# Performance work log

Hardware: AMD Instinct MI355X
Metric: run time of the kernel (lower is better)

## Reference

```python
import jax, jax.numpy as jnp
import numpy as np

B, S, DIN, H, N, L_S4, L_RES, ED = 512, 500, 14, 128, 256, 4, 6, 256


def setup_inputs() -> dict:
    key = jax.random.key(0)
    ks = jax.random.split(key, 32)
    f = jnp.float32
    rn = lambda k, sh, s: jax.random.normal(k, sh, f) * s
    inp = {
        'x': rn(ks[0], (B, S, DIN), 1.0),
        'timesteps': jax.random.randint(ks[1], (B,), 0, 1000),
        'mask': (jax.random.uniform(ks[2], (B, S, 1)) < 0.9).astype(f),
        'observed': rn(ks[3], (B, S, DIN), 1.0),
        'W_in': rn(ks[4], (DIN, H), DIN ** -0.5), 'b_in': jnp.zeros((H,), f),
        'time_W1': rn(ks[5], (ED, 2 * H), ED ** -0.5), 'time_b1': jnp.zeros((2 * H,), f),
        'time_W2': rn(ks[6], (2 * H, H), (2 * H) ** -0.5), 'time_b2': jnp.zeros((H,), f),
        's4_ln_g': jnp.ones((L_S4, H), f), 's4_ln_b': jnp.zeros((L_S4, H), f),
        's4_logA': jnp.log(0.5 * jnp.ones((L_S4, H, N), f)),
        's4_Aim': jnp.broadcast_to(np.pi * jnp.arange(N, dtype=f), (L_S4, H, N)).copy(),
        's4_Cre': rn(ks[7], (L_S4, H, N), 0.5 ** 0.5),
        's4_Cim': rn(ks[8], (L_S4, H, N), 0.5 ** 0.5),
        's4_D': rn(ks[9], (L_S4, H), 1.0),
        's4_logdt': jax.random.uniform(ks[10], (L_S4, H), f, np.log(0.001), np.log(0.1)),
        's4_Wo': rn(ks[11], (L_S4, H, H), H ** -0.5), 's4_bo': jnp.zeros((L_S4, H), f),
        'res_ln_g': jnp.ones((L_RES, H), f), 'res_ln_b': jnp.zeros((L_RES, H), f),
        'res_W1': rn(ks[12], (L_RES, H, 2 * H), H ** -0.5), 'res_b1': jnp.zeros((L_RES, 2 * H), f),
        'res_W2': rn(ks[13], (L_RES, 2 * H, H), (2 * H) ** -0.5), 'res_b2': jnp.zeros((L_RES, H), f),
        'W_out': rn(ks[14], (H, DIN), H ** -0.5), 'b_out': jnp.zeros((DIN,), f),
    }
    return inp


def _ln(x, g, b):
    m = x.mean(-1, keepdims=True)
    v = ((x - m) ** 2).mean(-1, keepdims=True)
    return (x - m) * jax.lax.rsqrt(v + 1e-5) * g + b


def reference(x, timesteps, mask, observed, W_in, b_in, time_W1, time_b1, time_W2,
              time_b2, s4_ln_g, s4_ln_b, s4_logA, s4_Aim, s4_Cre, s4_Cim, s4_D,
              s4_logdt, s4_Wo, s4_bo, res_ln_g, res_ln_b, res_W1, res_b1, res_W2,
              res_b2, W_out, b_out):
    Bb, Ss, _ = x.shape
    Hh = W_in.shape[1]
    x_cond = x * mask + observed
    # sinusoidal positional encoding gated by mask -> [B,S,H]
    pos = jnp.arange(Ss, dtype=jnp.float32)
    div = jnp.exp(-jnp.log(10000.0) * 2.0 * jnp.arange(Hh // 2, dtype=jnp.float32) / Hh)
    ang = pos[:, None] * div
    pe = jnp.concatenate([jnp.sin(ang), jnp.cos(ang)], -1)  # [S,H]
    h = x_cond @ W_in + b_in + pe[None] * mask
    # S4D layers: prenorm -> FFT causal conv with Vandermonde kernel -> GELU -> proj -> residual
    t_idx = jnp.arange(Ss, dtype=jnp.float32)
    for l in range(s4_logA.shape[0]):
        z = _ln(h, s4_ln_g[l], s4_ln_b[l])
        dt = jnp.exp(s4_logdt[l])[:, None]                       # [H,1]
        A = -jnp.exp(s4_logA[l]) + 1j * s4_Aim[l]                # [H,N]
        dtA = dt * A
        C = (s4_Cre[l] + 1j * s4_Cim[l]) * (jnp.exp(dtA) - 1.0) / A
        V = jnp.exp(dtA[:, :, None] * t_idx)                     # [H,N,S]
        K = 2.0 * jnp.einsum('hn,hnl->hl', C, V).real            # [H,S]
        u = jnp.transpose(z, (0, 2, 1))                          # [B,H,S]
        n = 2 * Ss
        y = jnp.fft.irfft(jnp.fft.rfft(u, n) * jnp.fft.rfft(K, n), n)[..., :Ss]
        y = y + s4_D[l][None, :, None] * u
        y = jax.nn.gelu(jnp.transpose(y, (0, 2, 1)), approximate=False)
        h = h + y @ s4_Wo[l] + s4_bo[l]
    # diffusion time embedding
    half = time_W1.shape[0] // 2
    emb = jnp.log(10000.0) / (half - 1)
    freqs = jnp.exp(-emb * jnp.arange(half, dtype=jnp.float32))
    te = timesteps.astype(jnp.float32)[:, None] * freqs
    te = jnp.concatenate([jnp.sin(te), jnp.cos(te)], -1)
    te = jax.nn.silu(te @ time_W1 + time_b1) @ time_W2 + time_b2
    h = h + te[:, None, :]
    # residual MLP blocks
    for l in range(res_W1.shape[0]):
        z = _ln(h, res_ln_g[l], res_ln_b[l])
        h = h + jax.nn.gelu(z @ res_W1[l] + res_b1[l], approximate=False) @ res_W2[l] + res_b2[l]
    return h @ W_out + b_out
```

## Files before the change

### kernel.cpp

```cpp
#include <hip/hip_runtime.h>
#include <math.h>

#define B_ 512
#define S_ 500
#define SP_ 512
#define DIN_ 14
#define H_ 128
#define N_ 256
#define NT_ 256000

#define SWZ(r) ((((r) ^ ((r) >> 4)) & 15) << 4)

typedef __attribute__((ext_vector_type(8))) short short8v;
typedef __attribute__((ext_vector_type(4))) float f32x4;

__device__ __forceinline__ float gelu_f(float x) {
    float y = 0.7978845608028654f * x * (1.0f + 0.044715f * x * x);
    float t = 1.0f - __fdividef(2.0f, 1.0f + __expf(2.0f * y));
    return 0.5f * x * (1.0f + t);
}
__device__ __forceinline__ short f2bf(float f) {
    unsigned u = __builtin_bit_cast(unsigned, f);
    u += 0x7fffu + ((u >> 16) & 1u);
    return (short)(u >> 16);
}
__device__ __forceinline__ float bf2f(short s) {
    return __builtin_bit_cast(float, ((unsigned)(unsigned short)s) << 16);
}

__global__ __launch_bounds__(256) void k_kmat(
    const float* __restrict__ logA, const float* __restrict__ Aim,
    const float* __restrict__ Cre, const float* __restrict__ Cim,
    const float* __restrict__ logdt, float* __restrict__ Km)
{
    int lh = blockIdx.x;
    __shared__ float sCr[256], sCi[256], sAr[256], sAif[256];
    {
        int n = threadIdx.x;
        int idx = lh * N_ + n;
        double dt  = exp((double)logdt[lh]);
        double Are = -exp((double)logA[idx]);
        double Aiv = (double)Aim[idx];
        double ar  = dt * Are, ai = dt * Aiv;
        double er  = exp(ar);
        double E1r = er * cos(ai) - 1.0, E1i = er * sin(ai);
        double inv = 1.0 / (Are * Are + Aiv * Aiv);
        double qR  = (E1r * Are + E1i * Aiv) * inv;
        double qI  = (E1i * Are - E1r * Aiv) * inv;
        double cre = (double)Cre[idx], cim = (double)Cim[idx];
        sCr[n] = (float)(cre * qR - cim * qI);
        sCi[n] = (float)(cre * qI + cim * qR);
        sAr[n] = (float)ar;
        sAif[n] = (float)fmod(ai, 6.283185307179586476925286766559);
    }
    __syncthreads();
    for (int s = threadIdx.x; s < SP_; s += 256) {
        float acc = 0.0f;
        if (s < S_) {
            float fs = (float)s;
            for (int n = 0; n < N_; ++n) {
                float er = __expf(sAr[n] * fs);
                float y = sAif[n] * fs;
                y -= 6.28318530717958648f * rintf(y * 0.159154943091895336f);
                float sn, cs; __sincosf(y, &sn, &cs);
                acc = fmaf(er * sCr[n], cs, acc);
                acc = fmaf(-er * sCi[n], sn, acc);
            }
            acc *= 2.0f;
        }
        Km[lh * SP_ + s] = acc;
    }
}

__global__ __launch_bounds__(256) void k_toep(
    const float* __restrict__ Kl, short* __restrict__ Tblk)
{
    int hh = blockIdx.x, d = blockIdx.y;
    const float* Kr = Kl + hh * SP_;
    short* Tb = Tblk + (((size_t)hh * 4 + d) << 14);
    int base = d * 128;
    for (int i = threadIdx.x; i < 16384; i += 256) {
        int s = i >> 7, t = i & 127;
        int diff = base + s - t;
        float v = (diff >= 0 && diff < S_) ? Kr[diff] : 0.f;
        Tb[i] = f2bf(v);
    }
}

__global__ __launch_bounds__(128) void k_petab(float* __restrict__ pet)
{
    int s = blockIdx.x, j = threadIdx.x;
    int jj = j & 63;
    float dv = expf(-0.14391156831212787f * (float)jj);
    float ang = (float)s * dv;
    pet[s * 128 + j] = (j < 64) ? sinf(ang) : cosf(ang);
}

__global__ __launch_bounds__(256) void k_inproj(
    const float* __restrict__ x, const float* __restrict__ mask,
    const float* __restrict__ obs, const float* __restrict__ Win,
    const float* __restrict__ bin, const float* __restrict__ pet,
    float* __restrict__ h, float2* __restrict__ st)
{
    int wid = threadIdx.x >> 6, lane = threadIdx.x & 63;
    int tok0 = blockIdx.x * 16 + wid * 4;
    float w0[DIN_], w1[DIN_];
#pragma unroll
    for (int d = 0; d < DIN_; ++d) {
        w0[d] = Win[d * H_ + lane];
        w1[d] = Win[d * H_ + lane + 64];
    }
    float b0 = bin[lane], b1 = bin[lane + 64];
    for (int t = 0; t < 4; ++t) {
        int tok = tok0 + t;
        int s = tok % S_;
        float m = mask[tok];
        float a0 = b0, a1 = b1;
        const float* xp = x + (size_t)tok * DIN_;
        const float* op = obs + (size_t)tok * DIN_;
#pragma unroll
        for (int d = 0; d < DIN_; ++d) {
            float xc = xp[d] * m + op[d];
            a0 += xc * w0[d];
            a1 += xc * w1[d];
        }
        float h0 = a0 + pet[s * 128 + lane] * m;
        float h1 = a1 + pet[s * 128 + lane + 64] * m;
        float s1 = h0 + h1, s2 = h0 * h0 + h1 * h1;
#pragma unroll
        for (int off = 32; off > 0; off >>= 1) {
            s1 += __shfl_xor(s1, off, 64);
            s2 += __shfl_xor(s2, off, 64);
        }
        float mu = s1 * 0.0078125f;
        float rs = rsqrtf(s2 * 0.0078125f - mu * mu + 1e-5f);
        if (lane == 0) st[tok] = make_float2(mu, rs);
        h[(size_t)tok * H_ + lane] = h0;
        h[(size_t)tok * H_ + lane + 64] = h1;
    }
}

__global__ __launch_bounds__(256) void k_temb(
    const int* __restrict__ ts, const float* __restrict__ W1,
    const float* __restrict__ b1, const float* __restrict__ W2,
    const float* __restrict__ b2, float* __restrict__ te)
{
    __shared__ float feat[256];
    __shared__ float mid[256];
    int b = blockIdx.x, j = threadIdx.x;
    float t = (float)ts[b];
    float fr = expf(-0.07252236513367075f * (float)(j & 127));
    float ang = t * fr;
    feat[j] = (j < 128) ? sinf(ang) : cosf(ang);
    __syncthreads();
    float acc = b1[j];
    for (int k = 0; k < 256; ++k) acc += feat[k] * W1[k * 256 + j];
    mid[j] = acc / (1.0f + expf(-acc));
    __syncthreads();
    if (j < 128) {
        float a2 = b2[j];
        for (int k = 0; k < 256; ++k) a2 += mid[k] * W2[k * 128 + j];
        te[b * 128 + j] = a2;
    }
}

__global__ __launch_bounds__(256) void k_wcast(
    const float* __restrict__ Wo, const float* __restrict__ rW1,
    const float* __restrict__ rW2,
    short* __restrict__ WoT, short* __restrict__ W1T, short* __restrict__ W2T)
{
    int i = blockIdx.x * 256 + threadIdx.x;
    if (i < 65536) {
        int l = i >> 14, r = i & 16383, n = r >> 7, k = r & 127;
        WoT[i] = f2bf(Wo[(size_t)(l * 128 + k) * 128 + n]);
    } else if (i < 262144) {
        int j = i - 65536;
        int l = j >> 15, r = j & 32767, n = r >> 7, k = r & 127;
        W1T[j] = f2bf(rW1[(size_t)(l * 128 + k) * 256 + n]);
    } else if (i < 458752) {
        int j = i - 262144;
        int l = j >> 15, r = j & 32767, n = r >> 8, k = r & 255;
        W2T[j] = f2bf(rW2[(size_t)(l * 256 + k) * 128 + n]);
    }
}

__global__ __launch_bounds__(256) void k_ln_tb(
    const float* __restrict__ h, const float2* __restrict__ stc,
    const float* __restrict__ g, const float* __restrict__ be,
    short* __restrict__ ubt)
{
    int b = blockIdx.x, s0 = blockIdx.y * 64;
    int ntok = min(64, S_ - s0);
    __shared__ float tile[64 * 129];
    __shared__ float mu_[64], rs_[64];
    for (int idx = threadIdx.x; idx < (ntok << 7); idx += 256) {
        int i = idx >> 7, k = idx & 127;
        tile[i * 129 + k] = h[(size_t)(b * S_ + s0 + i) * H_ + k];
    }
    if (threadIdx.x < ntok) {
        float2 ms = stc[(size_t)b * S_ + s0 + threadIdx.x];
        mu_[threadIdx.x] = ms.x; rs_[threadIdx.x] = ms.y;
    }
    __syncthreads();
    for (int idx = threadIdx.x; idx < 128 * 32; idx += 256) {
        int k = idx >> 5, i = (idx & 31) * 2;
        float v0 = (i < ntok)     ? (tile[i * 129 + k]       - mu_[i])     * rs_[i]     * g[k] + be[k] : 0.f;
        float v1 = (i + 1 < ntok) ? (tile[(i + 1) * 129 + k] - mu_[i + 1]) * rs_[i + 1] * g[k] + be[k] : 0.f;
        unsigned lo = (unsigned short)f2bf(v0);
        unsigned hi = (unsigned short)f2bf(v1);
        *(unsigned*)(ubt + ((size_t)b * H_ + k) * SP_ + s0 + i) = lo | (hi << 16);
    }
}

__global__ __launch_bounds__(256) void k_cgemm(
    const short* __restrict__ ubt, const short* __restrict__ Tblk,
    const float* __restrict__ D, short* __restrict__ ybt)
{
    __shared__ short As[16384];
    __shared__ short Bs[16384];
    int hh = blockIdx.x, si = blockIdx.y, bt = blockIdx.z;
    int tid = threadIdx.x;
    int lane = tid & 63, wid = tid >> 6;
    int wm = wid >> 1, wn = wid & 1;
    int fr = lane & 15, ko = (lane >> 4) << 3;
    const short* Ab = ubt + ((size_t)(bt * 128) * H_ + hh) * SP_;

    f32x4 acc[4][4];
    f32x4 zv = {0.f, 0.f, 0.f, 0.f};
#pragma unroll
    for (int m = 0; m < 4; ++m)
#pragma unroll
        for (int n = 0; n < 4; ++n) acc[m][n] = zv;

    for (int tj = 0; tj <= si; ++tj) {
        if (tj) __syncthreads();
        const short* Bb = Tblk + (((size_t)hh * 4 + (si - tj)) << 14);
#pragma unroll
        for (int p = 0; p < 8; ++p) {
            int idx = p * 256 + tid;
            int row = idx >> 4, c16 = idx & 15;
            int byt = row * 256 + ((c16 * 16) ^ SWZ(row));
            *(short8v*)((char*)As + byt) =
                *(const short8v*)(Ab + (size_t)row * (H_ * SP_) + tj * 128 + c16 * 8);
            *(short8v*)((char*)Bs + byt) =
                *(const short8v*)(Bb + row * 128 + c16 * 8);
        }
        __syncthreads();
#pragma unroll
        for (int ks = 0; ks < 4; ++ks) {
            short8v a[4], b[4];
#pragma unroll
            for (int m = 0; m < 4; ++m) {
                int row = wm * 64 + m * 16 + fr;
                int byt = row * 256 + (((ks * 32 + ko) * 2) ^ SWZ(row));
                a[m] = *(const short8v*)((const char*)As + byt);
            }
#pragma unroll
            for (int n = 0; n < 4; ++n) {
                int row = wn * 64 + n * 16 + fr;
                int byt = row * 256 + (((ks * 32 + ko) * 2) ^ SWZ(row));
                b[n] = *(const short8v*)((const char*)Bs + byt);
            }
#pragma unroll
            for (int m = 0; m < 4; ++m)
#pragma unroll
                for (int n = 0; n < 4; ++n)
                    acc[m][n] = __builtin_amdgcn_mfma_f32_16x16x32_bf16(
                        a[m], b[n], acc[m][n], 0, 0, 0);
        }
        if (tj < si) __syncthreads();
    }

    float Dh = D[hh];
#pragma unroll
    for (int m = 0; m < 4; ++m) {
        int b0 = wm * 64 + m * 16 + (lane >> 4) * 4;
#pragma unroll
        for (int n = 0; n < 4; ++n) {
            int sC = si * 128 + wn * 64 + n * 16 + fr;
#pragma unroll
            for (int j = 0; j < 4; ++j) {
                int bg = bt * 128 + b0 + j;
                size_t off = ((size_t)bg * H_ + hh) * SP_ + sC;
                float u = bf2f(ubt[off]);
                ybt[off] = f2bf(gelu_f(acc[m][n][j] + Dh * u));
            }
        }
    }
}

__global__ __launch_bounds__(256) void k_p4(
    const short* __restrict__ ybt, const short* __restrict__ BT,
    const float* __restrict__ bias, const float* __restrict__ te,
    float* __restrict__ hres, float2* __restrict__ st,
    short* __restrict__ un, const float* __restrict__ gn,
    const float* __restrict__ bn)
{
    __shared__ __align__(16) char smem[65536];
    int tid = threadIdx.x;
    int bm = blockIdx.x;
    int bl = bm >> 2, s0t = (bm & 3) * 128;
    int lane = tid & 63, wid = tid >> 6;
    int wm = wid >> 1, wn = wid & 1;
    int fr = lane & 15, ko = (lane >> 4) << 3;

    f32x4 acc[4][4];
    f32x4 zv = {0.f, 0.f, 0.f, 0.f};
#pragma unroll
    for (int m = 0; m < 4; ++m)
#pragma unroll
        for (int n = 0; n < 4; ++n) acc[m][n] = zv;

    const short* Yb = ybt + ((size_t)bl << 16);
#pragma unroll
    for (int p = 0; p < 8; ++p) {
        int idx = p * 256 + tid;
        int hh = idx >> 4, sc = idx & 15;
        short8v y = *(const short8v*)(Yb + (size_t)hh * 512 + s0t + sc * 8);
#pragma unroll
        for (int e = 0; e < 8; ++e) {
            int row = sc * 8 + e;
            int byt = row * 256 + ((hh * 2) ^ SWZ(row));
            *(short*)(smem + byt) = y[e];
        }
    }
#pragma unroll
    for (int p = 0; p < 8; ++p) {
        int idx = p * 256 + tid;
        int row = idx >> 4, c16 = idx & 15;
        int byt = row * 256 + ((c16 * 16) ^ SWZ(row));
        *(short8v*)(smem + 32768 + byt) =
            *(const short8v*)(BT + (size_t)row * 128 + c16 * 8);
    }
    __syncthreads();
#pragma unroll
    for (int ks = 0; ks < 4; ++ks) {
        short8v a[4], b[4];
#pragma unroll
        for (int m = 0; m < 4; ++m) {
            int row = wm * 64 + m * 16 + fr;
            int byt = row * 256 + (((ks * 32 + ko) * 2) ^ SWZ(row));
            a[m] = *(const short8v*)(smem + byt);
        }
#pragma unroll
        for (int n = 0; n < 4; ++n) {
            int row = wn * 64 + n * 16 + fr;
            int byt = row * 256 + (((ks * 32 + ko) * 2) ^ SWZ(row));
            b[n] = *(const short8v*)(smem + 32768 + byt);
        }
#pragma unroll
        for (int m = 0; m < 4; ++m)
#pragma unroll
            for (int n = 0; n < 4; ++n)
                acc[m][n] = __builtin_amdgcn_mfma_f32_16x16x32_bf16(
                    a[m], b[n], acc[m][n], 0, 0, 0);
    }

    float* red = (float*)smem;
    short* znT = (short*)(smem + 32768);
    __syncthreads();
#pragma unroll
    for (int m = 0; m < 4; ++m) {
#pragma unroll
        for (int j = 0; j < 4; ++j) {
            int rl = wm * 64 + m * 16 + (lane >> 4) * 4 + j;
            int R = bm * 128 + rl;
            int b_ = R >> 9, s = R & 511;
            bool valid = (s < S_);
            float s1 = 0.f, s2 = 0.f;
#pragma unroll
            for (int n = 0; n < 4; ++n) {
                int C = wn * 64 + n * 16 + fr;
                float v = 0.f;
                if (valid) {
                    float t = te ? te[b_ * 128 + C] : 0.f;
                    size_t go = ((size_t)b_ * S_ + s) * 128 + C;
                    v = hres[go] + acc[m][n][j] + bias[C] + t;
                    hres[go] = v;
                }
                acc[m][n][j] = v;
                s1 += v; s2 += v * v;
            }
            s1 += __shfl_xor(s1, 1, 64); s2 += __shfl_xor(s2, 1, 64);
            s1 += __shfl_xor(s1, 2, 64); s2 += __shfl_xor(s2, 2, 64);
            s1 += __shfl_xor(s1, 4, 64); s2 += __shfl_xor(s2, 4, 64);
            s1 += __shfl_xor(s1, 8, 64); s2 += __shfl_xor(s2, 8, 64);
            if (fr == 0) {
                red[(wn * 128 + rl) * 2]     = s1;
                red[(wn * 128 + rl) * 2 + 1] = s2;
            }
        }
    }
    __syncthreads();
#pragma unroll
    for (int m = 0; m < 4; ++m) {
#pragma unroll
        for (int j = 0; j < 4; ++j) {
            int rl = wm * 64 + m * 16 + (lane >> 4) * 4 + j;
            int R = bm * 128 + rl;
            int b_ = R >> 9, s = R & 511;
            bool valid = (s < S_);
            float s1 = red[rl * 2]     + red[(128 + rl) * 2];
            float s2 = red[rl * 2 + 1] + red[(128 + rl) * 2 + 1];
            float mu = s1 * 0.0078125f;
            float rs = rsqrtf(s2 * 0.0078125f - mu * mu + 1e-5f);
            if (valid && fr == 0 && wn == 0)
                st[(size_t)b_ * S_ + s] = make_float2(mu, rs);
            if (un) {
#pragma unroll
                for (int n = 0; n < 4; ++n) {
                    int C = wn * 64 + n * 16 + fr;
                    float z = valid ? (acc[m][n][j] - mu) * rs * gn[C] + bn[C] : 0.f;
                    *(short*)((char*)znT + C * 256 + ((rl * 2) ^ SWZ(C))) = f2bf(z);
                }
            }
        }
    }
    if (un) {
        __syncthreads();
#pragma unroll
        for (int p = 0; p < 8; ++p) {
            int idx = p * 256 + tid;
            int C = idx >> 4, rlg = idx & 15;
            short8v z8 = *(const short8v*)((const char*)znT + C * 256 + ((rlg * 16) ^ SWZ(C)));
            *(short8v*)(un + (((size_t)(bl * 128 + C)) << 9) + s0t + rlg * 8) = z8;
        }
    }
}

__global__ __launch_bounds__(512) void k_mlp(
    float* hres, const float2* __restrict__ st,
    const short* __restrict__ W1T, const float* __restrict__ rb1,
    const short* __restrict__ W2T, const float* __restrict__ rb2,
    const float* __restrict__ g6, const float* __restrict__ b6)
{
    __shared__ __align__(16) char As1[32768];
    __shared__ __align__(16) char BsA[32768];
    int tid = threadIdx.x;
    int lane = tid & 63, wid = tid >> 6;
    int wm = wid >> 1, wn = wid & 1;
    int fr = lane & 15, ko = (lane >> 4) << 3;
    int q4 = (lane >> 4) * 4;
    size_t tok0 = (size_t)blockIdx.x * 128;

    f32x4 v[2][4];
#pragma unroll
    for (int m = 0; m < 2; ++m) {
#pragma unroll
        for (int j = 0; j < 4; ++j) {
            int rl = wm * 32 + m * 16 + q4 + j;
            float2 ms = st[tok0 + rl];
            const float* hp = hres + (tok0 + rl) * 128;
#pragma unroll
            for (int n = 0; n < 4; ++n) {
                int C = wn * 64 + n * 16 + fr;
                float hv = hp[C];
                v[m][n][j] = hv;
                float z = (hv - ms.x) * ms.y * g6[C] + b6[C];
                int byt = rl * 256 + ((C * 2) ^ SWZ(rl));
                *(short*)(As1 + byt) = f2bf(z);
            }
        }
    }

    for (int l = 0; l < 6; ++l) {
        const short* W1 = W1T + l * 32768;
        const short* W2 = W2T + l * 32768;
        const float* b1 = rb1 + l * 256;
        const float* b2 = rb2 + l * 128;

        f32x4 acc1[2][8];
        f32x4 zvv = {0.f, 0.f, 0.f, 0.f};
#pragma unroll
        for (int m = 0; m < 2; ++m)
#pragma unroll
            for (int n = 0; n < 8; ++n) acc1[m][n] = zvv;

#pragma unroll
        for (int gy = 0; gy < 2; ++gy) {
#pragma unroll
            for (int p = 0; p < 4; ++p) {
                int idx = p * 512 + tid;
                int row = idx >> 4, c16 = idx & 15;
                int byt = row * 256 + ((c16 * 16) ^ SWZ(row));
                *(short8v*)(BsA + byt) =
                    *(const short8v*)(W1 + (size_t)(gy * 128 + row) * 128 + c16 * 8);
            }
            __syncthreads();
#pragma unroll
            for (int ks = 0; ks < 4; ++ks) {
                short8v a[2], b[4];
#pragma unroll
                for (int m = 0; m < 2; ++m) {
                    int row = wm * 32 + m * 16 + fr;
                    int byt = row * 256 + (((ks * 32 + ko) * 2) ^ SWZ(row));
                    a[m] = *(const short8v*)(As1 + byt);
                }
#pragma unroll
                for (int n = 0; n < 4; ++n) {
                    int row = wn * 64 + n * 16 + fr;
                    int byt = row * 256 + (((ks * 32 + ko) * 2) ^ SWZ(row));
                    b[n] = *(const short8v*)(BsA + byt);
                }
#pragma unroll
                for (int m = 0; m < 2; ++m)
#pragma unroll
                    for (int n = 0; n < 4; ++n)
                        acc1[m][gy * 4 + n] = __builtin_amdgcn_mfma_f32_16x16x32_bf16(
                            a[m], b[n], acc1[m][gy * 4 + n], 0, 0, 0);
            }
            __syncthreads();
        }

        f32x4 acc2[2][4];
#pragma unroll
        for (int m = 0; m < 2; ++m)
#pragma unroll
            for (int n = 0; n < 4; ++n) acc2[m][n] = zvv;
#pragma unroll
        for (int kk = 0; kk < 2; ++kk) {
#pragma unroll
            for (int m = 0; m < 2; ++m) {
#pragma unroll
                for (int j = 0; j < 4; ++j) {
                    int rl = wm * 32 + m * 16 + q4 + j;
#pragma unroll
                    for (int n = 0; n < 4; ++n) {
                        int c = wn * 64 + n * 16 + fr;
                        float y1 = gelu_f(acc1[m][kk * 4 + n][j] + b1[kk * 128 + c]);
                        int byt = rl * 256 + ((c * 2) ^ SWZ(rl));
                        *(short*)(As1 + byt) = f2bf(y1);
                    }
                }
            }
#pragma unroll
            for (int p = 0; p < 4; ++p) {
                int idx = p * 512 + tid;
                int row = idx >> 4, c16 = idx & 15;
                int byt = row * 256 + ((c16 * 16) ^ SWZ(row));
                *(short8v*)(BsA + byt) =
                    *(const short8v*)(W2 + (size_t)row * 256 + kk * 128 + c16 * 8);
            }
            __syncthreads();
#pragma unroll
            for (int ks = 0; ks < 4; ++ks) {
                short8v a[2], b[4];
#pragma unroll
                for (int m = 0; m < 2; ++m) {
                    int row = wm * 32 + m * 16 + fr;
                    int byt = row * 256 + (((ks * 32 + ko) * 2) ^ SWZ(row));
                    a[m] = *(const short8v*)(As1 + byt);
                }
#pragma unroll
                for (int n = 0; n < 4; ++n) {
                    int row = wn * 64 + n * 16 + fr;
                    int byt = row * 256 + (((ks * 32 + ko) * 2) ^ SWZ(row));
                    b[n] = *(const short8v*)(BsA + byt);
                }
#pragma unroll
                for (int m = 0; m < 2; ++m)
#pragma unroll
                    for (int n = 0; n < 4; ++n)
                        acc2[m][n] = __builtin_amdgcn_mfma_f32_16x16x32_bf16(
                            a[m], b[n], acc2[m][n], 0, 0, 0);
            }
            __syncthreads();
        }

#pragma unroll
        for (int m = 0; m < 2; ++m)
#pragma unroll
            for (int n = 0; n < 4; ++n) {
                float bj = b2[wn * 64 + n * 16 + fr];
#pragma unroll
                for (int j = 0; j < 4; ++j)
                    v[m][n][j] += acc2[m][n][j] + bj;
            }
        if (l < 5) {
            float* red = (float*)BsA;
#pragma unroll
            for (int m = 0; m < 2; ++m) {
#pragma unroll
                for (int j = 0; j < 4; ++j) {
                    int rl = wm * 32 + m * 16 + q4 + j;
                    float s1 = 0.f, s2 = 0.f;
#pragma unroll
                    for (int n = 0; n < 4; ++n) {
                        float t = v[m][n][j];
                        s1 += t; s2 += t * t;
                    }
                    s1 += __shfl_xor(s1, 1, 64); s2 += __shfl_xor(s2, 1, 64);
                    s1 += __shfl_xor(s1, 2, 64); s2 += __shfl_xor(s2, 2, 64);
                    s1 += __shfl_xor(s1, 4, 64); s2 += __shfl_xor(s2, 4, 64);
                    s1 += __shfl_xor(s1, 8, 64); s2 += __shfl_xor(s2, 8, 64);
                    if (fr == 0) {
                        red[(wn * 128 + rl) * 2]     = s1;
                        red[(wn * 128 + rl) * 2 + 1] = s2;
                    }
                }
            }
            __syncthreads();
            const float* gl = g6 + (l + 1) * 128;
            const float* bl2 = b6 + (l + 1) * 128;
#pragma unroll
            for (int m = 0; m < 2; ++m) {
#pragma unroll
                for (int j = 0; j < 4; ++j) {
                    int rl = wm * 32 + m * 16 + q4 + j;
                    float s1 = red[rl * 2]     + red[(128 + rl) * 2];
                    float s2 = red[rl * 2 + 1] + red[(128 + rl) * 2 + 1];
                    float mu = s1 * 0.0078125f;
                    float rs = rsqrtf(s2 * 0.0078125f - mu * mu + 1e-5f);
#pragma unroll
                    for (int n = 0; n < 4; ++n) {
                        int C = wn * 64 + n * 16 + fr;
                        float z = (v[m][n][j] - mu) * rs * gl[C] + bl2[C];
                        int byt = rl * 256 + ((C * 2) ^ SWZ(rl));
                        *(short*)(As1 + byt) = f2bf(z);
                    }
                }
            }
            __syncthreads();
        }
    }

#pragma unroll
    for (int m = 0; m < 2; ++m) {
#pragma unroll
        for (int j = 0; j < 4; ++j) {
            int rl = wm * 32 + m * 16 + q4 + j;
            float* hp = hres + (tok0 + rl) * 128;
#pragma unroll
            for (int n = 0; n < 4; ++n)
                hp[wn * 64 + n * 16 + fr] = v[m][n][j];
        }
    }
}

__global__ __launch_bounds__(256) void k_out(
    const float* __restrict__ h, const float* __restrict__ Wout,
    const float* __restrict__ bout, float* __restrict__ out)
{
    __shared__ float wt[16 * 132];
    __shared__ float tile[64 * 132];
    int tok0 = blockIdx.x * 64;
    for (int idx = threadIdx.x; idx < 2048; idx += 256) {
        int j = idx >> 7, k = idx & 127;
        wt[j * 132 + k] = (j < 14) ? Wout[k * 14 + j] : 0.f;
    }
    const float4* hp = (const float4*)(h + (size_t)tok0 * 128);
    for (int idx = threadIdx.x; idx < 2048; idx += 256) {
        int row = idx >> 5, c4 = idx & 31;
        *((float4*)(tile + row * 132) + c4) = hp[idx];
    }
    __syncthreads();
    int i = threadIdx.x >> 2, jq = threadIdx.x & 3;
    float aj[4] = {0.f, 0.f, 0.f, 0.f};
    const float4* tr = (const float4*)(tile + i * 132);
#pragma unroll 8
    for (int kk = 0; kk < 32; ++kk) {
        float4 hv = tr[kk];
#pragma unroll
        for (int r = 0; r < 4; ++r) {
            float4 wv = *((const float4*)(wt + (jq * 4 + r) * 132) + kk);
            aj[r] += hv.x * wv.x + hv.y * wv.y + hv.z * wv.z + hv.w * wv.w;
        }
    }
#pragma unroll
    for (int r = 0; r < 4; ++r) {
        int j = jq * 4 + r;
        if (j < 14)
            out[(size_t)(tok0 + i) * 14 + j] = aj[r] + bout[j];
    }
}

extern "C" void kernel_launch(void* const* d_in, const int* in_sizes, int n_in,
                              void* d_out, int out_size, void* d_ws, size_t ws_size,
                              hipStream_t stream)
{
    (void)in_sizes; (void)n_in; (void)out_size;
    const float* x      = (const float*)d_in[0];
    const int*   tsteps = (const int*)  d_in[1];
    const float* mask   = (const float*)d_in[2];
    const float* obs    = (const float*)d_in[3];
    const float* Win    = (const float*)d_in[4];
    const float* bin    = (const float*)d_in[5];
    const float* tW1    = (const float*)d_in[6];
    const float* tb1    = (const float*)d_in[7];
    const float* tW2    = (const float*)d_in[8];
    const float* tb2    = (const float*)d_in[9];
    const float* lng4   = (const float*)d_in[10];
    const float* lnb4   = (const float*)d_in[11];
    const float* logA   = (const float*)d_in[12];
    const float* Aim    = (const float*)d_in[13];
    const float* Cre    = (const float*)d_in[14];
    const float* Cim    = (const float*)d_in[15];
    const float* Dp     = (const float*)d_in[16];
    const float* logdt  = (const float*)d_in[17];
    const float* Wo     = (const float*)d_in[18];
    const float* bo     = (const float*)d_in[19];
    const float* lng6   = (const float*)d_in[20];
    const float* lnb6   = (const float*)d_in[21];
    const float* rW1    = (const float*)d_in[22];
    const float* rb1    = (const float*)d_in[23];
    const float* rW2    = (const float*)d_in[24];
    const float* rb2    = (const float*)d_in[25];
    const float* Woutp  = (const float*)d_in[26];
    const float* boutp  = (const float*)d_in[27];

    float*  ws  = (float*)d_ws;
    float*  h   = ws;
    float*  Km  = h + 32768000;
    float*  te  = Km + 262144;
    float2* st  = (float2*)(te + 65536);
    float*  pet = (float*)st + 512000;
    short*  WoT = (short*)(pet + 64000);
    short*  W1T = WoT + 65536;
    short*  W2T = W1T + 196608;
    float*  big = (float*)(W2T + 196608);
    size_t  wf  = ws_size / sizeof(float);
    size_t  fixed = 33901056;
    size_t  avail = (wf > fixed) ? (wf - fixed) : 0;

    bool flowA = (avail >= 29360128);

    k_kmat<<<512, 256, 0, stream>>>(logA, Aim, Cre, Cim, logdt, Km);
    k_petab<<<S_, 128, 0, stream>>>(pet);
    k_inproj<<<NT_ / 16, 256, 0, stream>>>(x, mask, obs, Win, bin, pet, h, st);
    k_temb<<<B_, 256, 0, stream>>>(tsteps, tW1, tb1, tW2, tb2, te);
    k_wcast<<<1792, 256, 0, stream>>>(Wo, rW1, rW2, WoT, W1T, W2T);

    if (flowA) {
        short* ubtA = (short*)big;
        short* ubtB = ubtA + 16777216;
        short* ybt  = ubtB + 16777216;
        short* Tblk = ybt + 16777216;

        k_ln_tb<<<dim3(256, 8), 256, 0, stream>>>(h, st, lng4, lnb4, ubtA);
        k_ln_tb<<<dim3(256, 8), 256, 0, stream>>>(
            h + (size_t)256 * S_ * H_, st + (size_t)256 * S_, lng4, lnb4, ubtB);

        for (int l = 0; l < 4; ++l) {
            k_toep<<<dim3(H_, 4), 256, 0, stream>>>(Km + (size_t)l * H_ * SP_, Tblk);
            for (int cb = 0; cb < 2; ++cb) {
                size_t bOff = (size_t)cb * 256;
                float* hb = h + bOff * S_ * H_;
                short* ub = cb ? ubtB : ubtA;
                const float* tep = (l == 3) ? (te + bOff * H_) : (const float*)0;
                short* un = (l < 3) ? ub : (short*)0;
                k_cgemm<<<dim3(H_, 4, 2), 256, 0, stream>>>(ub, Tblk, Dp + l * H_, ybt);
                k_p4<<<1024, 256, 0, stream>>>(
                    ybt, WoT + l * 16384, bo + l * H_, tep, hb, st + bOff * S_,
                    un, lng4 + (l + 1) * H_, lnb4 + (l + 1) * H_);
            }
        }
    } else {
        int CHB = 64;
        for (int c = 256; c >= 64; c >>= 1)
            if ((size_t)c * 65536 + 4194304 <= avail) { CHB = c; break; }
        short* ubt  = (short*)big;
        short* ybt  = ubt + (size_t)CHB * 65536;
        short* Tblk = ybt + (size_t)CHB * 65536;
        int nCB = B_ / CHB;
        for (int l = 0; l < 4; ++l) {
            k_toep<<<dim3(H_, 4), 256, 0, stream>>>(Km + (size_t)l * H_ * SP_, Tblk);
            for (int cb = 0; cb < nCB; ++cb) {
                size_t bOff = (size_t)cb * CHB;
                float* hb = h + bOff * S_ * H_;
                const float* tep = (l == 3) ? (te + bOff * H_) : (const float*)0;
                k_ln_tb<<<dim3(CHB, 8), 256, 0, stream>>>(
                    hb, st + bOff * S_, lng4 + l * H_, lnb4 + l * H_, ubt);
                k_cgemm<<<dim3(H_, 4, CHB / 128), 256, 0, stream>>>(
                    ubt, Tblk, Dp + l * H_, ybt);
                k_p4<<<CHB * 4, 256, 0, stream>>>(
                    ybt, WoT + l * 16384, bo + l * H_, tep, hb, st + bOff * S_,
                    (short*)0, lng4, lnb4);
            }
        }
    }

    k_mlp<<<NT_ / 128, 512, 0, stream>>>(h, st, W1T, rb1, W2T, rb2, lng6, lnb6);

    k_out<<<NT_ / 64, 256, 0, stream>>>(h, Woutp, boutp, (float*)d_out);
}
```

Measured before the change: 2.078 ms.

## Swap MFMA operand roles in residual MLP so each lane owns contiguous features

The residual MLP kernel now feeds weights as the A operand and tokens as the B operand of the MFMA. Each lane's accumulator then holds four consecutive feature columns for one token. This allows vectorised float4 global loads and stores of the residual state, short4 LDS writes of the LayerNorm and GELU outputs, and float4 loads of biases and LN parameters, replacing scattered scalar accesses. The LN row reduction shrinks to two cross-lane shuffles per token. The cost is a different LDS access pattern that must stay conflict-free under the existing swizzle.

```diff
diff --git a/kernel.cpp b/kernel.cpp
--- a/kernel.cpp
+++ b/kernel.cpp
@@ -12,6 +12,7 @@
 #define SWZ(r) ((((r) ^ ((r) >> 4)) & 15) << 4)
 
 typedef __attribute__((ext_vector_type(8))) short short8v;
+typedef __attribute__((ext_vector_type(4))) short short4v;
 typedef __attribute__((ext_vector_type(4))) float f32x4;
 
 __device__ __forceinline__ float gelu_f(float x) {
@@ -438,43 +439,47 @@
     __shared__ __align__(16) char BsA[32768];
     int tid = threadIdx.x;
     int lane = tid & 63, wid = tid >> 6;
-    int wm = wid >> 1, wn = wid & 1;
-    int fr = lane & 15, ko = (lane >> 4) << 3;
-    int q4 = (lane >> 4) * 4;
+    int tq = wid >> 1, cq = wid & 1;
+    int fr = lane & 15, q = lane >> 4;
+    int ko = q * 8, q4 = q * 4;
     size_t tok0 = (size_t)blockIdx.x * 128;
 
-    f32x4 v[2][4];
-#pragma unroll
-    for (int m = 0; m < 2; ++m) {
-#pragma unroll
-        for (int j = 0; j < 4; ++j) {
-            int rl = wm * 32 + m * 16 + q4 + j;
-            float2 ms = st[tok0 + rl];
-            const float* hp = hres + (tok0 + rl) * 128;
-#pragma unroll
-            for (int n = 0; n < 4; ++n) {
-                int C = wn * 64 + n * 16 + fr;
-                float hv = hp[C];
-                v[m][n][j] = hv;
-                float z = (hv - ms.x) * ms.y * g6[C] + b6[C];
-                int byt = rl * 256 + ((C * 2) ^ SWZ(rl));
-                *(short*)(As1 + byt) = f2bf(z);
-            }
+    f32x4 v[4][2];
+    f32x4 zvv = {0.f, 0.f, 0.f, 0.f};
+
+#pragma unroll
+    for (int nn = 0; nn < 2; ++nn) {
+        int tok = tq * 32 + nn * 16 + fr;
+        float2 ms = st[tok0 + tok];
+        const float* hp = hres + (tok0 + tok) * 128;
+#pragma unroll
+        for (int m2 = 0; m2 < 4; ++m2) {
+            int cb = m2 * 32 + cq * 16 + q4;
+            float4 hv = *(const float4*)(hp + cb);
+            v[m2][nn][0] = hv.x; v[m2][nn][1] = hv.y;
+            v[m2][nn][2] = hv.z; v[m2][nn][3] = hv.w;
+            float4 gv = *(const float4*)(g6 + cb);
+            float4 bv = *(const float4*)(b6 + cb);
+            short4v z;
+            z[0] = f2bf((hv.x - ms.x) * ms.y * gv.x + bv.x);
+            z[1] = f2bf((hv.y - ms.x) * ms.y * gv.y + bv.y);
+            z[2] = f2bf((hv.z - ms.x) * ms.y * gv.z + bv.z);
+            z[3] = f2bf((hv.w - ms.x) * ms.y * gv.w + bv.w);
+            *(short4v*)(As1 + tok * 256 + ((cb * 2) ^ SWZ(tok))) = z;
         }
     }
 
     for (int l = 0; l < 6; ++l) {
         const short* W1 = W1T + l * 32768;
         const short* W2 = W2T + l * 32768;
-        const float* b1 = rb1 + l * 256;
-        const float* b2 = rb2 + l * 128;
-
-        f32x4 acc1[2][8];
-        f32x4 zvv = {0.f, 0.f, 0.f, 0.f};
-#pragma unroll
-        for (int m = 0; m < 2; ++m)
-#pragma unroll
-            for (int n = 0; n < 8; ++n) acc1[m][n] = zvv;
+
+        f32x4 acc1[2][4][2];
+#pragma unroll
+        for (int gy = 0; gy < 2; ++gy)
+#pragma unroll
+            for (int m1 = 0; m1 < 4; ++m1)
+#pragma unroll
+                for (int nn = 0; nn < 2; ++nn) acc1[gy][m1][nn] = zvv;
 
 #pragma unroll
         for (int gy = 0; gy < 2; ++gy) {
@@ -489,48 +494,45 @@
             __syncthreads();
 #pragma unroll
             for (int ks = 0; ks < 4; ++ks) {
-                short8v a[2], b[4];
-#pragma unroll
-                for (int m = 0; m < 2; ++m) {
-                    int row = wm * 32 + m * 16 + fr;
-                    int byt = row * 256 + (((ks * 32 + ko) * 2) ^ SWZ(row));
-                    a[m] = *(const short8v*)(As1 + byt);
-                }
-#pragma unroll
-                for (int n = 0; n < 4; ++n) {
-                    int row = wn * 64 + n * 16 + fr;
-                    int byt = row * 256 + (((ks * 32 + ko) * 2) ^ SWZ(row));
-                    b[n] = *(const short8v*)(BsA + byt);
-                }
-#pragma unroll
-                for (int m = 0; m < 2; ++m)
-#pragma unroll
-                    for (int n = 0; n < 4; ++n)
-                        acc1[m][gy * 4 + n] = __builtin_amdgcn_mfma_f32_16x16x32_bf16(
-                            a[m], b[n], acc1[m][gy * 4 + n], 0, 0, 0);
+                short8v b[2];
+#pragma unroll
+                for (int nn = 0; nn < 2; ++nn) {
+                    int row = tq * 32 + nn * 16 + fr;
+                    b[nn] = *(const short8v*)(As1 + row * 256 + (((ks * 32 + ko) * 2) ^ SWZ(row)));
+                }
+#pragma unroll
+                for (int m1 = 0; m1 < 4; ++m1) {
+                    int row = m1 * 32 + cq * 16 + fr;
+                    short8v a = *(const short8v*)(BsA + row * 256 + (((ks * 32 + ko) * 2) ^ SWZ(row)));
+#pragma unroll
+                    for (int nn = 0; nn < 2; ++nn)
+                        acc1[gy][m1][nn] = __builtin_amdgcn_mfma_f32_16x16x32_bf16(
+                            a, b[nn], acc1[gy][m1][nn], 0, 0, 0);
+                }
             }
             __syncthreads();
         }
 
-        f32x4 acc2[2][4];
-#pragma unroll
-        for (int m = 0; m < 2; ++m)
-#pragma unroll
-            for (int n = 0; n < 4; ++n) acc2[m][n] = zvv;
+        f32x4 acc2[4][2];
+#pragma unroll
+        for (int m2 = 0; m2 < 4; ++m2)
+#pragma unroll
+            for (int nn = 0; nn < 2; ++nn) acc2[m2][nn] = zvv;
 #pragma unroll
         for (int kk = 0; kk < 2; ++kk) {
 #pragma unroll
-            for (int m = 0; m < 2; ++m) {
-#pragma unroll
-                for (int j = 0; j < 4; ++j) {
-                    int rl = wm * 32 + m * 16 + q4 + j;
-#pragma unroll
-                    for (int n = 0; n < 4; ++n) {
-                        int c = wn * 64 + n * 16 + fr;
-                        float y1 = gelu_f(acc1[m][kk * 4 + n][j] + b1[kk * 128 + c]);
-                        int byt = rl * 256 + ((c * 2) ^ SWZ(rl));
-                        *(short*)(As1 + byt) = f2bf(y1);
-                    }
+            for (int m1 = 0; m1 < 4; ++m1) {
+                int nb = m1 * 32 + cq * 16 + q4;
+                float4 bv = *(const float4*)(rb1 + l * 256 + kk * 128 + nb);
+#pragma unroll
+                for (int nn = 0; nn < 2; ++nn) {
+                    int tok = tq * 32 + nn * 16 + fr;
+                    short4v mz;
+                    mz[0] = f2bf(gelu_f(acc1[kk][m1][nn][0] + bv.x));
+                    mz[1] = f2bf(gelu_f(acc1[kk][m1][nn][1] + bv.y));
+                    mz[2] = f2bf(gelu_f(acc1[kk][m1][nn][2] + bv.z));
+                    mz[3] = f2bf(gelu_f(acc1[kk][m1][nn][3] + bv.w));
+                    *(short4v*)(As1 + tok * 256 + ((nb * 2) ^ SWZ(tok))) = mz;
                 }
             }
 #pragma unroll
@@ -544,80 +546,80 @@
             __syncthreads();
 #pragma unroll
             for (int ks = 0; ks < 4; ++ks) {
-                short8v a[2], b[4];
-#pragma unroll
-                for (int m = 0; m < 2; ++m) {
-                    int row = wm * 32 + m * 16 + fr;
-                    int byt = row * 256 + (((ks * 32 + ko) * 2) ^ SWZ(row));
-                    a[m] = *(const short8v*)(As1 + byt);
-                }
-#pragma unroll
-                for (int n = 0; n < 4; ++n) {
-                    int row = wn * 64 + n * 16 + fr;
-                    int byt = row * 256 + (((ks * 32 + ko) * 2) ^ SWZ(row));
-                    b[n] = *(const short8v*)(BsA + byt);
-                }
-#pragma unroll
-                for (int m = 0; m < 2; ++m)
-#pragma unroll
-                    for (int n = 0; n < 4; ++n)
-                        acc2[m][n] = __builtin_amdgcn_mfma_f32_16x16x32_bf16(
-                            a[m], b[n], acc2[m][n], 0, 0, 0);
+                short8v b[2];
+#pragma unroll
+                for (int nn = 0; nn < 2; ++nn) {
+                    int row = tq * 32 + nn * 16 + fr;
+                    b[nn] = *(const short8v*)(As1 + row * 256 + (((ks * 32 + ko) * 2) ^ SWZ(row)));
+                }
+#pragma unroll
+                for (int m2 = 0; m2 < 4; ++m2) {
+                    int row = m2 * 32 + cq * 16 + fr;
+                    short8v a = *(const short8v*)(BsA + row * 256 + (((ks * 32 + ko) * 2) ^ SWZ(row)));
+#pragma unroll
+                    for (int nn = 0; nn < 2; ++nn)
+                        acc2[m2][nn] = __builtin_amdgcn_mfma_f32_16x16x32_bf16(
+                            a, b[nn], acc2[m2][nn], 0, 0, 0);
+                }
             }
             __syncthreads();
         }
 
 #pragma unroll
-        for (int m = 0; m < 2; ++m)
-#pragma unroll
-            for (int n = 0; n < 4; ++n) {
-                float bj = b2[wn * 64 + n * 16 + fr];
-#pragma unroll
-                for (int j = 0; j < 4; ++j)
-                    v[m][n][j] += acc2[m][n][j] + bj;
-            }
+        for (int m2 = 0; m2 < 4; ++m2) {
+            int cb = m2 * 32 + cq * 16 + q4;
+            float4 b2v = *(const float4*)(rb2 + l * 128 + cb);
+#pragma unroll
+            for (int nn = 0; nn < 2; ++nn) {
+                v[m2][nn][0] += acc2[m2][nn][0] + b2v.x;
+                v[m2][nn][1] += acc2[m2][nn][1] + b2v.y;
+                v[m2][nn][2] += acc2[m2][nn][2] + b2v.z;
+                v[m2][nn][3] += acc2[m2][nn][3] + b2v.w;
+            }
+        }
         if (l < 5) {
             float* red = (float*)BsA;
-#pragma unroll
-            for (int m = 0; m < 2; ++m) {
-#pragma unroll
-                for (int j = 0; j < 4; ++j) {
-                    int rl = wm * 32 + m * 16 + q4 + j;
-                    float s1 = 0.f, s2 = 0.f;
-#pragma unroll
-                    for (int n = 0; n < 4; ++n) {
-                        float t = v[m][n][j];
-                        s1 += t; s2 += t * t;
+            float s1[2] = {0.f, 0.f}, s2[2] = {0.f, 0.f};
+#pragma unroll
+            for (int nn = 0; nn < 2; ++nn) {
+#pragma unroll
+                for (int m2 = 0; m2 < 4; ++m2)
+#pragma unroll
+                    for (int j = 0; j < 4; ++j) {
+                        float t = v[m2][nn][j];
+                        s1[nn] += t; s2[nn] += t * t;
                     }
-                    s1 += __shfl_xor(s1, 1, 64); s2 += __shfl_xor(s2, 1, 64);
-                    s1 += __shfl_xor(s1, 2, 64); s2 += __shfl_xor(s2, 2, 64);
-                    s1 += __shfl_xor(s1, 4, 64); s2 += __shfl_xor(s2, 4, 64);
-                    s1 += __shfl_xor(s1, 8, 64); s2 += __shfl_xor(s2, 8, 64);
-                    if (fr == 0) {
-                        red[(wn * 128 + rl) * 2]     = s1;
-                        red[(wn * 128 + rl) * 2 + 1] = s2;
-                    }
+                s1[nn] += __shfl_xor(s1[nn], 16, 64);
+                s1[nn] += __shfl_xor(s1[nn], 32, 64);
+                s2[nn] += __shfl_xor(s2[nn], 16, 64);
+                s2[nn] += __shfl_xor(s2[nn], 32, 64);
+                if (q == 0) {
+                    int tok = tq * 32 + nn * 16 + fr;
+                    red[tok * 2 + cq] = s1[nn];
+                    red[256 + tok * 2 + cq] = s2[nn];
                 }
             }
             __syncthreads();
             const float* gl = g6 + (l + 1) * 128;
             const float* bl2 = b6 + (l + 1) * 128;
 #pragma unroll
-            for (int m = 0; m < 2; ++m) {
-#pragma unroll
-                for (int j = 0; j < 4; ++j) {
-                    int rl = wm * 32 + m * 16 + q4 + j;
-                    float s1 = red[rl * 2]     + red[(128 + rl) * 2];
-                    float s2 = red[rl * 2 + 1] + red[(128 + rl) * 2 + 1];
-                    float mu = s1 * 0.0078125f;
-                    float rs = rsqrtf(s2 * 0.0078125f - mu * mu + 1e-5f);
-#pragma unroll
-                    for (int n = 0; n < 4; ++n) {
-                        int C = wn * 64 + n * 16 + fr;
-                        float z = (v[m][n][j] - mu) * rs * gl[C] + bl2[C];
-                        int byt = rl * 256 + ((C * 2) ^ SWZ(rl));
-                        *(short*)(As1 + byt) = f2bf(z);
-                    }
+            for (int nn = 0; nn < 2; ++nn) {
+                int tok = tq * 32 + nn * 16 + fr;
+                float S1 = red[tok * 2] + red[tok * 2 + 1];
+                float S2 = red[256 + tok * 2] + red[256 + tok * 2 + 1];
+                float mu = S1 * 0.0078125f;
+                float rs = rsqrtf(S2 * 0.0078125f - mu * mu + 1e-5f);
+#pragma unroll
+                for (int m2 = 0; m2 < 4; ++m2) {
+                    int cb = m2 * 32 + cq * 16 + q4;
+                    float4 gv = *(const float4*)(gl + cb);
+                    float4 bv = *(const float4*)(bl2 + cb);
+                    short4v z;
+                    z[0] = f2bf((v[m2][nn][0] - mu) * rs * gv.x + bv.x);
+                    z[1] = f2bf((v[m2][nn][1] - mu) * rs * gv.y + bv.y);
+                    z[2] = f2bf((v[m2][nn][2] - mu) * rs * gv.z + bv.z);
+                    z[3] = f2bf((v[m2][nn][3] - mu) * rs * gv.w + bv.w);
+                    *(short4v*)(As1 + tok * 256 + ((cb * 2) ^ SWZ(tok))) = z;
                 }
             }
             __syncthreads();
@@ -625,14 +627,16 @@
     }
 
 #pragma unroll
-    for (int m = 0; m < 2; ++m) {
-#pragma unroll
-        for (int j = 0; j < 4; ++j) {
-            int rl = wm * 32 + m * 16 + q4 + j;
-            float* hp = hres + (tok0 + rl) * 128;
-#pragma unroll
-            for (int n = 0; n < 4; ++n)
-                hp[wn * 64 + n * 16 + fr] = v[m][n][j];
+    for (int nn = 0; nn < 2; ++nn) {
+        int tok = tq * 32 + nn * 16 + fr;
+        float* hp = hres + (tok0 + tok) * 128;
+#pragma unroll
+        for (int m2 = 0; m2 < 4; ++m2) {
+            int cb = m2 * 32 + cq * 16 + q4;
+            float4 o;
+            o.x = v[m2][nn][0]; o.y = v[m2][nn][1];
+            o.z = v[m2][nn][2]; o.w = v[m2][nn][3];
+            *(float4*)(hp + cb) = o;
         }
     }
 }
```

After: 2.057 ms. No clear change (-1.0%).
